# Kernel optimization log

Measured on AMD Instinct MI355X. Metric: run time of the kernel, lower is better.

The kernel has to match this reference:

```python
import jax, jax.numpy as jnp
import numpy as np

D_MODEL = 1024
NUM_HEADS = 16
D_HEAD = D_MODEL // NUM_HEADS


def setup_inputs() -> dict:
    key = jax.random.key(0)
    ks = jax.random.split(key, 5)
    s = 1.0 / np.sqrt(D_MODEL)
    x = jax.random.normal(ks[0], (4, 2048, D_MODEL), dtype=jnp.float32)
    w_qkv = jax.random.uniform(ks[1], (D_MODEL, 3 * D_MODEL), jnp.float32, -s, s)
    b_qkv = jax.random.uniform(ks[2], (3 * D_MODEL,), jnp.float32, -s, s)
    w_out = jax.random.uniform(ks[3], (D_MODEL, D_MODEL), jnp.float32, -s, s)
    b_out = jax.random.uniform(ks[4], (D_MODEL,), jnp.float32, -s, s)
    return {"x": x, "w_qkv": w_qkv, "b_qkv": b_qkv, "w_out": w_out, "b_out": b_out}


def reference(x, w_qkv, b_qkv, w_out, b_out):
    B, L, D = x.shape
    qkv = x @ w_qkv + b_qkv  # [B, L, 3D]
    qkv = qkv.reshape(B, L, 3, NUM_HEADS, D_HEAD)
    q, k, v = qkv[:, :, 0], qkv[:, :, 1], qkv[:, :, 2]  # [B, L, H, Dh]
    scores = jnp.einsum("bqhd,bkhd->bhqk", q, k) / np.sqrt(D_HEAD).astype(np.float32)
    attn = jax.nn.softmax(scores, axis=-1)
    out = jnp.einsum("bhqk,bkhd->bqhd", attn, v).reshape(B, L, D)
    return out @ w_out + b_out
```

## Files before the change

### kernel.cpp

```cpp
#include <hip/hip_runtime.h>
#include <stdint.h>

typedef unsigned short u16;
typedef __attribute__((ext_vector_type(8))) short bh8;
typedef __attribute__((ext_vector_type(4))) float f4;

#define LOG2E 1.44269504088896f
#define QSCALE 0.18033688f

__device__ inline u16 f2bf(float f) {
  union { float f; uint32_t u; } c; c.f = f;
  uint32_t u = c.u;
  return (u16)((u + 0x7fffu + ((u >> 16) & 1u)) >> 16);
}

__device__ inline float fast_exp2(float x) {
#if __has_builtin(__builtin_amdgcn_exp2f)
  return __builtin_amdgcn_exp2f(x);
#else
  return exp2f(x);
#endif
}

#if __has_builtin(__builtin_amdgcn_global_load_lds)
#define GLD16(gp, lp) __builtin_amdgcn_global_load_lds( \
    (const __attribute__((address_space(1))) void*)(gp), \
    (__attribute__((address_space(3))) void*)(lp), 16, 0, 0)
#else
#define GLD16(gp, lp) do { *(bh8*)(lp) = *(const bh8*)(gp); } while (0)
#endif


__global__ __launch_bounds__(256) void cvt_f32_bf16(const float* __restrict__ src,
                                                    u16* __restrict__ dst, int n4) {
  int i = blockIdx.x * 256 + threadIdx.x;
  if (i < n4) {
    float4 v = ((const float4*)src)[i];
    ushort4 o;
    o.x = f2bf(v.x); o.y = f2bf(v.y); o.z = f2bf(v.z); o.w = f2bf(v.w);
    ((ushort4*)dst)[i] = o;
  }
}

__global__ __launch_bounds__(1024) void transpose_cvt(const float* __restrict__ src,
                                                      u16* __restrict__ dst, int K, int N) {
  __shared__ float tile[32][33];
  int n0 = blockIdx.x * 32, k0 = blockIdx.y * 32;
  int tx = threadIdx.x, ty = threadIdx.y;
  tile[ty][tx] = src[(size_t)(k0 + ty) * N + n0 + tx];
  __syncthreads();
  dst[(size_t)(n0 + ty) * K + k0 + tx] = f2bf(tile[tx][ty]);
}

__global__ __launch_bounds__(1024) void transpose_b16(const u16* __restrict__ src,
                                                      u16* __restrict__ dst) {
  __shared__ u16 t[32][33];
  int bh = blockIdx.z, l0 = blockIdx.y * 32, d0 = blockIdx.x * 32;
  int tx = threadIdx.x, ty = threadIdx.y;
  t[ty][tx] = src[((size_t)bh * 2048 + l0 + ty) * 64 + d0 + tx];
  __syncthreads();
  dst[((size_t)bh * 64 + d0 + ty) * 2048 + l0 + tx] = t[tx][ty];
}

__device__ inline void gemm_mainloop(const u16* __restrict__ A, const u16* __restrict__ Bt,
                                     int K, int m0, int n0,
                                     u16* As, u16* Bs, f4 acc[4][4]) {
  const int tid  = threadIdx.x;
  const int lane = tid & 63;
  const int quad = lane >> 4;
  const int ml   = lane & 15;
  const int wave = tid >> 6;
  const int wm   = (wave >> 1) * 64;
  const int wn   = (wave & 1) * 64;

#pragma unroll 1
  for (int k0 = 0; k0 < K; k0 += 64) {
#pragma unroll
    for (int r = 0; r < 4; ++r) {
      int chunk = r * 256 + tid;
      int row = chunk >> 3, cc = chunk & 7;
      int cg = cc ^ (row & 7);
      GLD16(A + (size_t)(m0 + row) * K + k0 + cg * 8, As + chunk * 8);
    }
#pragma unroll
    for (int r = 0; r < 4; ++r) {
      int chunk = r * 256 + tid;
      int row = chunk >> 3, cc = chunk & 7;
      int cg = cc ^ (row & 7);
      GLD16(Bt + (size_t)(n0 + row) * K + k0 + cg * 8, Bs + chunk * 8);
    }
    __syncthreads();
#pragma unroll
    for (int ks = 0; ks < 2; ++ks) {
      bh8 af[4], bfr[4];
      int cs = (ks * 4 + quad) ^ (ml & 7);
#pragma unroll
      for (int i = 0; i < 4; ++i) {
        int row = wm + i * 16 + ml;
        af[i] = *(const bh8*)(As + (row * 8 + cs) * 8);
      }
#pragma unroll
      for (int j = 0; j < 4; ++j) {
        int row = wn + j * 16 + ml;
        bfr[j] = *(const bh8*)(Bs + (row * 8 + cs) * 8);
      }
#pragma unroll
      for (int i = 0; i < 4; ++i)
#pragma unroll
        for (int j = 0; j < 4; ++j)
          acc[i][j] = __builtin_amdgcn_mfma_f32_16x16x32_bf16(af[i], bfr[j], acc[i][j], 0, 0, 0);
    }
    __syncthreads();
  }
}

__global__ __launch_bounds__(256) void gemm_qkv(const u16* __restrict__ xb,
                                                const u16* __restrict__ wqt,
                                                const float* __restrict__ bqkv,
                                                u16* __restrict__ q, u16* __restrict__ k,
                                                u16* __restrict__ v) {
  __shared__ __align__(16) u16 smem[2 * 128 * 64];
  const f4 fzero = {0.f, 0.f, 0.f, 0.f};
  f4 acc[4][4];
#pragma unroll
  for (int i = 0; i < 4; ++i)
#pragma unroll
    for (int j = 0; j < 4; ++j) acc[i][j] = fzero;

  int m0 = blockIdx.y * 128, n0 = blockIdx.x * 128;
  gemm_mainloop(xb, wqt, 1024, m0, n0, smem, smem + 128 * 64, acc);

  const int lane = threadIdx.x & 63, wave = threadIdx.x >> 6;
  const int quad = lane >> 4, ml = lane & 15;
  const int wm = (wave >> 1) * 64, wn = (wave & 1) * 64;
  u16* dst = (n0 < 1024) ? q : ((n0 < 2048) ? k : v);
  float scale = (n0 < 1024) ? QSCALE : 1.0f;
#pragma unroll
  for (int j = 0; j < 4; ++j) {
    int nn = n0 + wn + j * 16 + ml;
    int h = (nn >> 6) & 15, d = nn & 63;
    float bias = bqkv[nn];
#pragma unroll
    for (int i = 0; i < 4; ++i) {
#pragma unroll
      for (int r = 0; r < 4; ++r) {
        int tok = m0 + wm + i * 16 + quad * 4 + r;
        int b = tok >> 11, l = tok & 2047;
        int bh = b * 16 + h;
        dst[((size_t)bh * 2048 + l) * 64 + d] = f2bf((acc[i][j][r] + bias) * scale);
      }
    }
  }
}

__global__ __launch_bounds__(256) void gemm_out(const u16* __restrict__ ob,
                                                const u16* __restrict__ wot,
                                                const float* __restrict__ bout,
                                                float* __restrict__ out) {
  __shared__ __align__(16) u16 smem[2 * 128 * 64];
  const f4 fzero = {0.f, 0.f, 0.f, 0.f};
  f4 acc[4][4];
#pragma unroll
  for (int i = 0; i < 4; ++i)
#pragma unroll
    for (int j = 0; j < 4; ++j) acc[i][j] = fzero;

  int m0 = blockIdx.y * 128, n0 = blockIdx.x * 128;
  gemm_mainloop(ob, wot, 1024, m0, n0, smem, smem + 128 * 64, acc);

  const int lane = threadIdx.x & 63, wave = threadIdx.x >> 6;
  const int quad = lane >> 4, ml = lane & 15;
  const int wm = (wave >> 1) * 64, wn = (wave & 1) * 64;
#pragma unroll
  for (int j = 0; j < 4; ++j) {
    int nn = n0 + wn + j * 16 + ml;
    float bias = bout[nn];
#pragma unroll
    for (int i = 0; i < 4; ++i)
#pragma unroll
      for (int r = 0; r < 4; ++r) {
        int tok = m0 + wm + i * 16 + quad * 4 + r;
        out[(size_t)tok * 1024 + nn] = acc[i][j][r] + bias;
      }
  }
}

__global__ __launch_bounds__(256, 4) void attn(const u16* __restrict__ q,
                                               const u16* __restrict__ k,
                                               const u16* __restrict__ vt,
                                               u16* __restrict__ o) {
  __shared__ __align__(16) u16 Ks[2][64 * 64];
  __shared__ __align__(16) u16 Vs[2][64 * 64];
  __shared__ __align__(16) u16 Pq[4][16 * 64];
  const int bh = blockIdx.x;
  const int b = bh >> 4, h = bh & 15;
  const int tid = threadIdx.x;
  const int wave = tid >> 6, lane = tid & 63;
  const int quad = lane >> 4, ml = lane & 15;
  const int qw = blockIdx.y * 128 + wave * 32;
  const u16* qp = q + (size_t)bh * 2048 * 64;
  const u16* kp = k + (size_t)bh * 2048 * 64;
  const u16* vp = vt + (size_t)bh * 64 * 2048;
  const f4 fzero = {0.f, 0.f, 0.f, 0.f};

  const int mlx = ml & 7;
  const int mlsw = ml & 14;

  bh8 qf[2][2];
#pragma unroll
  for (int g = 0; g < 2; ++g)
#pragma unroll
    for (int ks = 0; ks < 2; ++ks)
      qf[g][ks] = *(const bh8*)&qp[(size_t)(qw + g * 16 + ml) * 64 + ks * 32 + quad * 8];

  f4 oacc[2][4];
#pragma unroll
  for (int g = 0; g < 2; ++g)
#pragma unroll
    for (int j = 0; j < 4; ++j) oacc[g][j] = fzero;
  float lsum[2] = {0.f, 0.f};

  const int srow = tid >> 3, scc = tid & 7;
  const int scg = scc ^ (srow & 7);
  u16* pq = &Pq[wave][ml * 64];

#pragma unroll
  for (int r = 0; r < 2; ++r) {
    int row = r * 32 + srow;
    GLD16(kp + (size_t)row * 64 + scg * 8, &Ks[0][(row * 8 + scc) * 8]);
    GLD16(vp + (size_t)row * 2048 + scg * 8, &Vs[0][(row * 8 + scc) * 8]);
  }
  __syncthreads();

  int cur = 0;
#pragma unroll 1
  for (int t = 0; t < 32; ++t) {
    if (t < 31) {
      int ktn = (t + 1) * 64;
#pragma unroll
      for (int r = 0; r < 2; ++r) {
        int row = r * 32 + srow;
        GLD16(kp + (size_t)(ktn + row) * 64 + scg * 8, &Ks[cur ^ 1][(row * 8 + scc) * 8]);
        GLD16(vp + (size_t)row * 2048 + ktn + scg * 8, &Vs[cur ^ 1][(row * 8 + scc) * 8]);
      }
    }

    f4 s[2][4];
#pragma unroll
    for (int g = 0; g < 2; ++g)
#pragma unroll
      for (int j = 0; j < 4; ++j) s[g][j] = fzero;
#pragma unroll
    for (int ks = 0; ks < 2; ++ks) {
      int cs = (ks * 4 + quad) ^ mlx;
      bh8 kf[4];
#pragma unroll
      for (int j = 0; j < 4; ++j)
        kf[j] = *(const bh8*)(&Ks[cur][((j * 16 + ml) * 8 + cs) * 8]);
#pragma unroll
      for (int j = 0; j < 4; ++j) {
        s[0][j] = __builtin_amdgcn_mfma_f32_16x16x32_bf16(kf[j], qf[0][ks], s[0][j], 0, 0, 0);
        s[1][j] = __builtin_amdgcn_mfma_f32_16x16x32_bf16(kf[j], qf[1][ks], s[1][j], 0, 0, 0);
      }
    }

#pragma unroll
    for (int ks = 0; ks < 2; ++ks) {
#pragma unroll
      for (int g = 0; g < 2; ++g) {
#pragma unroll
        for (int jl = 0; jl < 2; ++jl) {
          int j = ks * 2 + jl;
          uint32_t w[4];
#pragma unroll
          for (int r = 0; r < 4; ++r) {
            float p = fast_exp2(s[g][j][r]);
            union { float f; uint32_t u; } c; c.f = p;
            c.u = (c.u + 0x8000u) & 0xFFFF0000u;
            lsum[g] += c.f;
            w[r] = c.u;
          }
          uint2 pk;
          pk.x = (w[0] >> 16) | w[1];
          pk.y = (w[2] >> 16) | w[3];
          int u = g * 8 + jl * 4 + quad;
          *(uint2*)(pq + ((u ^ mlsw) << 2)) = pk;
        }
      }

      int cs = (ks * 4 + quad) ^ mlx;
      bh8 vf[4];
#pragma unroll
      for (int j = 0; j < 4; ++j)
        vf[j] = *(const bh8*)(&Vs[cur][((j * 16 + ml) * 8 + cs) * 8]);
#pragma unroll
      for (int g = 0; g < 2; ++g) {
        int u = g * 8 + 2 * quad;
        bh8 pf = *(const bh8*)(pq + ((u ^ mlsw) << 2));
#pragma unroll
        for (int j = 0; j < 4; ++j)
          oacc[g][j] = __builtin_amdgcn_mfma_f32_16x16x32_bf16(vf[j], pf, oacc[g][j], 0, 0, 0);
      }
    }
    __syncthreads();
    cur ^= 1;
  }

#pragma unroll
  for (int g = 0; g < 2; ++g) {
    lsum[g] += __shfl_xor(lsum[g], 16, 64);
    lsum[g] += __shfl_xor(lsum[g], 32, 64);
    float inv = 1.0f / lsum[g];
    size_t obase = (((size_t)b * 2048 + qw + g * 16 + ml) * 16 + h) * 64;
#pragma unroll
    for (int j = 0; j < 4; ++j) {
      ushort4 w;
      w.x = f2bf(oacc[g][j][0] * inv);
      w.y = f2bf(oacc[g][j][1] * inv);
      w.z = f2bf(oacc[g][j][2] * inv);
      w.w = f2bf(oacc[g][j][3] * inv);
      *(ushort4*)(o + obase + j * 16 + quad * 4) = w;
    }
  }
}


extern "C" void kernel_launch(void* const* d_in, const int* in_sizes, int n_in,
                              void* d_out, int out_size, void* d_ws, size_t ws_size,
                              hipStream_t stream) {
  const float* x     = (const float*)d_in[0];
  const float* w_qkv = (const float*)d_in[1];
  const float* b_qkv = (const float*)d_in[2];
  const float* w_out = (const float*)d_in[3];
  const float* b_out = (const float*)d_in[4];
  float* out = (float*)d_out;

  u16* ws  = (u16*)d_ws;
  u16* xb  = ws;
  u16* wqt = xb + (size_t)8192 * 1024;
  u16* wot = wqt + (size_t)3072 * 1024;
  u16* qb  = wot + (size_t)1024 * 1024;
  u16* kb  = qb + (size_t)64 * 2048 * 64;
  u16* vb  = kb + (size_t)64 * 2048 * 64;
  u16* vtb = xb;
  u16* ob  = vb;

  cvt_f32_bf16<<<8192, 256, 0, stream>>>(x, xb, 8192 * 1024 / 4);
  transpose_cvt<<<dim3(96, 32), dim3(32, 32), 0, stream>>>(w_qkv, wqt, 1024, 3072);
  transpose_cvt<<<dim3(32, 32), dim3(32, 32), 0, stream>>>(w_out, wot, 1024, 1024);
  gemm_qkv<<<dim3(24, 64), 256, 0, stream>>>(xb, wqt, b_qkv, qb, kb, vb);
  transpose_b16<<<dim3(2, 64, 64), dim3(32, 32), 0, stream>>>(vb, vtb);
  attn<<<dim3(64, 16), 256, 0, stream>>>(qb, kb, vtb, ob);
  gemm_out<<<dim3(8, 64), 256, 0, stream>>>(ob, wot, b_out, out);
}
```

Before: 289.3 us.

## Use 64x128 tiles for output GEMM and refine P LDS swizzle in attention

Replaces the 128x128 output-projection GEMM with a dedicated 64x128-tile kernel, doubling the grid to 1024 blocks so the 256 CUs get more blocks and better wave balance. The new kernel runs its own single-buffered loop through LDS, which may expose load latency compared with the shared mainloop. Separately, the attention kernel's P-tile LDS swizzle now XORs with the full lane index at 8-byte granularity and reads the MFMA operand as two 8-byte loads, aiming to reduce LDS bank conflicts at the cost of more load instructions.

```diff
diff --git a/kernel.cpp b/kernel.cpp
--- a/kernel.cpp
+++ b/kernel.cpp
@@ -153,30 +153,69 @@
   }
 }
 
-__global__ __launch_bounds__(256) void gemm_out(const u16* __restrict__ ob,
-                                                const u16* __restrict__ wot,
-                                                const float* __restrict__ bout,
-                                                float* __restrict__ out) {
-  __shared__ __align__(16) u16 smem[2 * 128 * 64];
+__global__ __launch_bounds__(256) void gemm_out64(const u16* __restrict__ ob,
+                                                  const u16* __restrict__ wot,
+                                                  const float* __restrict__ bout,
+                                                  float* __restrict__ out) {
+  __shared__ __align__(16) u16 As[64 * 64];
+  __shared__ __align__(16) u16 Bs[128 * 64];
+  const int tid  = threadIdx.x;
+  const int lane = tid & 63;
+  const int quad = lane >> 4;
+  const int ml   = lane & 15;
+  const int wave = tid >> 6;
+  const int wm   = (wave >> 1) * 32;
+  const int wn   = (wave & 1) * 64;
+  const int m0 = blockIdx.y * 64, n0 = blockIdx.x * 128;
+
   const f4 fzero = {0.f, 0.f, 0.f, 0.f};
-  f4 acc[4][4];
-#pragma unroll
-  for (int i = 0; i < 4; ++i)
+  f4 acc[2][4];
+#pragma unroll
+  for (int i = 0; i < 2; ++i)
 #pragma unroll
     for (int j = 0; j < 4; ++j) acc[i][j] = fzero;
 
-  int m0 = blockIdx.y * 128, n0 = blockIdx.x * 128;
-  gemm_mainloop(ob, wot, 1024, m0, n0, smem, smem + 128 * 64, acc);
-
-  const int lane = threadIdx.x & 63, wave = threadIdx.x >> 6;
-  const int quad = lane >> 4, ml = lane & 15;
-  const int wm = (wave >> 1) * 64, wn = (wave & 1) * 64;
+  const int srow = tid >> 3, scc = tid & 7;
+  const int scg = scc ^ (srow & 7);
+
+#pragma unroll 1
+  for (int k0 = 0; k0 < 1024; k0 += 64) {
+#pragma unroll
+    for (int r = 0; r < 2; ++r) {
+      int row = r * 32 + srow;
+      GLD16(ob + (size_t)(m0 + row) * 1024 + k0 + scg * 8, As + (row * 8 + scc) * 8);
+    }
+#pragma unroll
+    for (int r = 0; r < 4; ++r) {
+      int row = r * 32 + srow;
+      GLD16(wot + (size_t)(n0 + row) * 1024 + k0 + scg * 8, Bs + (row * 8 + scc) * 8);
+    }
+    __syncthreads();
+#pragma unroll
+    for (int ks = 0; ks < 2; ++ks) {
+      int cs = (ks * 4 + quad) ^ (ml & 7);
+      bh8 af[2], bfr[4];
+#pragma unroll
+      for (int i = 0; i < 2; ++i)
+        af[i] = *(const bh8*)(As + ((wm + i * 16 + ml) * 8 + cs) * 8);
+#pragma unroll
+      for (int j = 0; j < 4; ++j)
+        bfr[j] = *(const bh8*)(Bs + ((wn + j * 16 + ml) * 8 + cs) * 8);
+#pragma unroll
+      for (int i = 0; i < 2; ++i)
+#pragma unroll
+        for (int j = 0; j < 4; ++j)
+          acc[i][j] = __builtin_amdgcn_mfma_f32_16x16x32_bf16(af[i], bfr[j], acc[i][j], 0, 0, 0);
+    }
+    __syncthreads();
+  }
+
 #pragma unroll
   for (int j = 0; j < 4; ++j) {
     int nn = n0 + wn + j * 16 + ml;
     float bias = bout[nn];
 #pragma unroll
-    for (int i = 0; i < 4; ++i)
+    for (int i = 0; i < 2; ++i)
 #pragma unroll
       for (int r = 0; r < 4; ++r) {
         int tok = m0 + wm + i * 16 + quad * 4 + r;
@@ -204,7 +243,6 @@
   const f4 fzero = {0.f, 0.f, 0.f, 0.f};
 
   const int mlx = ml & 7;
-  const int mlsw = ml & 14;
 
   bh8 qf[2][2];
 #pragma unroll
@@ -283,8 +321,8 @@
           uint2 pk;
           pk.x = (w[0] >> 16) | w[1];
           pk.y = (w[2] >> 16) | w[3];
-          int u = g * 8 + jl * 4 + quad;
-          *(uint2*)(pq + ((u ^ mlsw) << 2)) = pk;
+          int sl = (g * 8 + jl * 4 + quad) ^ ml;
+          *(uint2*)(pq + (sl << 2)) = pk;
         }
       }
 
@@ -295,11 +333,15 @@
         vf[j] = *(const bh8*)(&Vs[cur][((j * 16 + ml) * 8 + cs) * 8]);
 #pragma unroll
       for (int g = 0; g < 2; ++g) {
-        int u = g * 8 + 2 * quad;
-        bh8 pf = *(const bh8*)(pq + ((u ^ mlsw) << 2));
+        int s0 = (g * 8 + 2 * quad) ^ ml;
+        int s1 = (g * 8 + 2 * quad + 1) ^ ml;
+        uint2 lo = *(const uint2*)(pq + (s0 << 2));
+        uint2 hi = *(const uint2*)(pq + (s1 << 2));
+        union { uint32_t u[4]; bh8 v; } pf;
+        pf.u[0] = lo.x; pf.u[1] = lo.y; pf.u[2] = hi.x; pf.u[3] = hi.y;
 #pragma unroll
         for (int j = 0; j < 4; ++j)
-          oacc[g][j] = __builtin_amdgcn_mfma_f32_16x16x32_bf16(vf[j], pf, oacc[g][j], 0, 0, 0);
+          oacc[g][j] = __builtin_amdgcn_mfma_f32_16x16x32_bf16(vf[j], pf.v, oacc[g][j], 0, 0, 0);
       }
     }
     __syncthreads();
@@ -351,5 +393,5 @@
   gemm_qkv<<<dim3(24, 64), 256, 0, stream>>>(xb, wqt, b_qkv, qb, kb, vb);
   transpose_b16<<<dim3(2, 64, 64), dim3(32, 32), 0, stream>>>(vb, vtb);
   attn<<<dim3(64, 16), 256, 0, stream>>>(qb, kb, vtb, ob);
-  gemm_out<<<dim3(8, 64), 256, 0, stream>>>(ob, wot, b_out, out);
-}
+  gemm_out64<<<dim3(8, 128), 256, 0, stream>>>(ob, wot, b_out, out);
+}
```

New measurement: 293.2 us. About the same (+1.3%).
